# Kernel optimization log

Measured on AMD Instinct MI355X. Metric: run time of the kernel, lower is better.

The kernel has to match this reference:

```python
import jax, jax.numpy as jnp
import numpy as np

B, N, D = 8, 512, 16


def setup_inputs() -> dict:
    key = jax.random.key(0)
    k1, k2 = jax.random.split(key)
    # Fully-connected adjacency with diagonal = -1 (self is excluded as neighbor),
    # matching the tf.where(adj != -1) -> reshape [-1, N, N-1] pattern.
    adj_matrix = jnp.where(jnp.eye(N, dtype=bool)[None, :, :], -1, 1)
    adj_matrix = jnp.broadcast_to(adj_matrix, (B, N, N)).astype(jnp.int64)
    adj_coef = jax.random.normal(k1, (B, N, N), dtype=jnp.float32)
    neighbour_messages = jax.random.normal(k2, (B, N, D), dtype=jnp.float32)
    return {
        "adj_matrix": adj_matrix,
        "adj_coef": adj_coef,
        "neighbour_messages": neighbour_messages,
    }


def reference(adj_matrix, adj_coef, neighbour_messages):
    b, n, d = neighbour_messages.shape
    # tf.where(adj != -1) enumerates, per row i (in ascending column order), the
    # N-1 valid neighbor columns. Reproduce jit-safely: push invalid cols to the
    # end with sentinel n, sort, keep first n-1.
    cols = jnp.arange(n)[None, None, :]
    valid = adj_matrix != -1
    neighbor_idx = jnp.sort(jnp.where(valid, cols, n), axis=-1)[..., : n - 1]  # [B,N,N-1]
    # Batched gather: [B,N,N-1,D]
    gathered = neighbour_messages[jnp.arange(b)[:, None, None], neighbor_idx]
    # Concat self features with neighbor features along the 'slot' axis -> [B,N,N,D]
    updated = jnp.concatenate([neighbour_messages[:, :, None, :], gathered], axis=2)
    # Weight each slot by its adjacency coefficient, then flatten slots*features.
    updated = adj_coef[..., None] * updated
    return updated.reshape(b, n, n * d)
```

## Files before the change

### kernel.cpp

```cpp
#include <hip/hip_runtime.h>

#define NN 512
#define DD 16

__global__ __launch_bounds__(512) void graph_layer_kernel(
    const int*    __restrict__ adj,
    const float*  __restrict__ coef,
    const float4* __restrict__ msg4,
    float4*       __restrict__ out4)
{
    __shared__ float4 smsg[NN * 4];
    __shared__ float  scoef[NN];
    __shared__ int    snb[NN];
    __shared__ int    wtot[8];

    const int row  = blockIdx.x;
    const int b    = row >> 9;
    const int i    = row & (NN - 1);
    const int t    = threadIdx.x;
    const int lane = t & 63;
    const int wv   = t >> 6;

    scoef[t] = coef[(size_t)row * NN + t];

    {
        const float4* src = msg4 + (size_t)b * (NN * 4);
        #pragma unroll
        for (int k = 0; k < 4; ++k)
            smsg[t + k * 512] = src[t + k * 512];
    }

    const int  a     = adj[(size_t)row * NN + t];
    const bool valid = (a != -1);
    const unsigned long long m = __ballot(valid);
    const int  rank  = __popcll(m & ((1ULL << lane) - 1ULL));
    snb[t] = NN - 1;
    if (lane == 0) wtot[wv] = __popcll(m);
    __syncthreads();

    int base = 0;
    #pragma unroll
    for (int w = 0; w < 8; ++w)
        base += (w < wv) ? wtot[w] : 0;
    if (valid) {
        const int pos = base + rank;
        if (pos < NN) snb[pos] = t;
    }
    __syncthreads();

    float4* orow = out4 + (size_t)row * (NN * 4);
    #pragma unroll
    for (int k = 0; k < 4; ++k) {
        const int g = t + k * 512;
        const int j = g >> 2;
        const int q = g & 3;
        const int s = (j == 0) ? i : snb[j - 1];
        const float c = scoef[j];
        const float4 v = smsg[s * 4 + q];
        float4 o;
        o.x = c * v.x; o.y = c * v.y; o.z = c * v.z; o.w = c * v.w;
        orow[g] = o;
    }
}

extern "C" void kernel_launch(void* const* d_in, const int* in_sizes, int n_in,
                              void* d_out, int out_size, void* d_ws, size_t ws_size,
                              hipStream_t stream) {
    const int*    adj  = (const int*)d_in[0];
    const float*  coef = (const float*)d_in[1];
    const float4* msg4 = (const float4*)d_in[2];
    float4*       out4 = (float4*)d_out;

    const int B = 8;
    graph_layer_kernel<<<B * NN, 512, 0, stream>>>(adj, coef, msg4, out4);
}
```

Baseline: 155.2 us.

## Drop shared memory staging; compute neighbor index per thread via ballot masks and select-bit

Removes the shared-memory staging of messages, coefficients and the neighbor list, along with both block barriers. Each wave now builds all eight ballot masks of the adjacency row, and each thread locates its neighbor column with prefix counts and a bitwise select. Messages and coefficients are read straight from global memory (L2-cached), and output is written with nontemporal stores. The cost is redundant adjacency loads per wave and more per-thread ALU work, in exchange for no LDS traffic, no block-wide sync and higher occupancy.

```diff
diff --git a/kernel.cpp b/kernel.cpp
--- a/kernel.cpp
+++ b/kernel.cpp
@@ -1,75 +1,88 @@
 #include <hip/hip_runtime.h>
 
 #define NN 512
-#define DD 16
+
+typedef float f4 __attribute__((ext_vector_type(4)));
+
+__device__ __forceinline__ int select_bit(unsigned long long m, int k) {
+    int pos = 0;
+    unsigned int w = (unsigned int)m;
+    int c = __popc(w);
+    if (k >= c) { k -= c; pos = 32; w = (unsigned int)(m >> 32); }
+    unsigned int h = w & 0xFFFFu; c = __popc(h);
+    if (k >= c) { k -= c; pos += 16; w >>= 16; }
+    h = w & 0xFFu; c = __popc(h);
+    if (k >= c) { k -= c; pos += 8; w >>= 8; }
+    h = w & 0xFu; c = __popc(h);
+    if (k >= c) { k -= c; pos += 4; w >>= 4; }
+    h = w & 0x3u; c = __popc(h);
+    if (k >= c) { k -= c; pos += 2; w >>= 2; }
+    if (k >= (int)(w & 0x1u)) pos += 1;
+    return pos;
+}
 
 __global__ __launch_bounds__(512) void graph_layer_kernel(
-    const int*    __restrict__ adj,
-    const float*  __restrict__ coef,
-    const float4* __restrict__ msg4,
-    float4*       __restrict__ out4)
+    const int*   __restrict__ adj,
+    const float* __restrict__ coef,
+    const f4*    __restrict__ msg4,
+    f4*          __restrict__ out4)
 {
-    __shared__ float4 smsg[NN * 4];
-    __shared__ float  scoef[NN];
-    __shared__ int    snb[NN];
-    __shared__ int    wtot[8];
-
     const int row  = blockIdx.x;
     const int b    = row >> 9;
     const int i    = row & (NN - 1);
     const int t    = threadIdx.x;
     const int lane = t & 63;
-    const int wv   = t >> 6;
+    const size_t rowbase = (size_t)row * NN;
 
-    scoef[t] = coef[(size_t)row * NN + t];
+    unsigned long long mask[8];
+    #pragma unroll
+    for (int c = 0; c < 8; ++c)
+        mask[c] = __ballot(adj[rowbase + c * 64 + lane] != -1);
 
-    {
-        const float4* src = msg4 + (size_t)b * (NN * 4);
-        #pragma unroll
-        for (int k = 0; k < 4; ++k)
-            smsg[t + k * 512] = src[t + k * 512];
-    }
+    int cum[9];
+    cum[0] = 0;
+    #pragma unroll
+    for (int c = 0; c < 8; ++c) cum[c + 1] = cum[c] + __popcll(mask[c]);
 
-    const int  a     = adj[(size_t)row * NN + t];
-    const bool valid = (a != -1);
-    const unsigned long long m = __ballot(valid);
-    const int  rank  = __popcll(m & ((1ULL << lane) - 1ULL));
-    snb[t] = NN - 1;
-    if (lane == 0) wtot[wv] = __popcll(m);
-    __syncthreads();
+    const f4* msgb = msg4 + (size_t)b * (NN * 4);
+    f4*       orow = out4 + (size_t)row * (NN * 4);
+    const int q = t & 3;
 
-    int base = 0;
-    #pragma unroll
-    for (int w = 0; w < 8; ++w)
-        base += (w < wv) ? wtot[w] : 0;
-    if (valid) {
-        const int pos = base + rank;
-        if (pos < NN) snb[pos] = t;
-    }
-    __syncthreads();
-
-    float4* orow = out4 + (size_t)row * (NN * 4);
     #pragma unroll
     for (int k = 0; k < 4; ++k) {
         const int g = t + k * 512;
         const int j = g >> 2;
-        const int q = g & 3;
-        const int s = (j == 0) ? i : snb[j - 1];
-        const float c = scoef[j];
-        const float4 v = smsg[s * 4 + q];
-        float4 o;
-        o.x = c * v.x; o.y = c * v.y; o.z = c * v.z; o.w = c * v.w;
-        orow[g] = o;
+
+        int s;
+        if (j == 0) {
+            s = i;
+        } else {
+            const int p = j - 1;
+            if (p >= cum[8]) {
+                s = NN - 1;
+            } else {
+                int c = 0;
+                #pragma unroll
+                for (int cc = 1; cc < 8; ++cc) c += (p >= cum[cc]) ? 1 : 0;
+                s = c * 64 + select_bit(mask[c], p - cum[c]);
+            }
+        }
+
+        const float cv = coef[rowbase + j];
+        const f4    v  = msgb[s * 4 + q];
+        f4 o;
+        o.x = cv * v.x; o.y = cv * v.y; o.z = cv * v.z; o.w = cv * v.w;
+        __builtin_nontemporal_store(o, orow + g);
     }
 }
 
 extern "C" void kernel_launch(void* const* d_in, const int* in_sizes, int n_in,
                               void* d_out, int out_size, void* d_ws, size_t ws_size,
                               hipStream_t stream) {
-    const int*    adj  = (const int*)d_in[0];
-    const float*  coef = (const float*)d_in[1];
-    const float4* msg4 = (const float4*)d_in[2];
-    float4*       out4 = (float4*)d_out;
+    const int*   adj  = (const int*)d_in[0];
+    const float* coef = (const float*)d_in[1];
+    const f4*    msg4 = (const f4*)d_in[2];
+    f4*          out4 = (f4*)d_out;
 
     const int B = 8;
     graph_layer_kernel<<<B * NN, 512, 0, stream>>>(adj, coef, msg4, out4);
```

New measurement: 168.0 us. 8.2% more time.

## Split neighbor compaction and weighted write into two kernels with nontemporal stores

Applied to the files above, without the earlier changes.

The fused kernel becomes two kernels. The first compacts each row's valid neighbor indices (with the self index at slot 0) into a workspace buffer. The second reads those indices, the coefficients and the messages straight from global memory, with no shared-memory staging of the 32KB message block per row, and writes the output with nontemporal stores. The aim is to drop the per-block shared-memory fill and the barriers and to keep the large output stream out of the caches, at the cost of an extra kernel launch and a round trip of the index buffer through global memory.

```diff
diff --git a/kernel.cpp b/kernel.cpp
--- a/kernel.cpp
+++ b/kernel.cpp
@@ -1,76 +1,82 @@
 #include <hip/hip_runtime.h>
 
 #define NN 512
-#define DD 16
 
-__global__ __launch_bounds__(512) void graph_layer_kernel(
-    const int*    __restrict__ adj,
-    const float*  __restrict__ coef,
-    const float4* __restrict__ msg4,
-    float4*       __restrict__ out4)
+typedef float f4 __attribute__((ext_vector_type(4)));
+
+__global__ __launch_bounds__(512) void compact_kernel(
+    const int* __restrict__ adj,
+    int*       __restrict__ sidx)
 {
-    __shared__ float4 smsg[NN * 4];
-    __shared__ float  scoef[NN];
-    __shared__ int    snb[NN];
-    __shared__ int    wtot[8];
-
+    __shared__ int wtot[8];
     const int row  = blockIdx.x;
-    const int b    = row >> 9;
     const int i    = row & (NN - 1);
     const int t    = threadIdx.x;
     const int lane = t & 63;
     const int wv   = t >> 6;
 
-    scoef[t] = coef[(size_t)row * NN + t];
-
-    {
-        const float4* src = msg4 + (size_t)b * (NN * 4);
-        #pragma unroll
-        for (int k = 0; k < 4; ++k)
-            smsg[t + k * 512] = src[t + k * 512];
-    }
-
-    const int  a     = adj[(size_t)row * NN + t];
-    const bool valid = (a != -1);
+    const bool valid = (adj[(size_t)row * NN + t] != -1);
     const unsigned long long m = __ballot(valid);
-    const int  rank  = __popcll(m & ((1ULL << lane) - 1ULL));
-    snb[t] = NN - 1;
+    const int rank = __popcll(m & ((1ULL << lane) - 1ULL));
     if (lane == 0) wtot[wv] = __popcll(m);
     __syncthreads();
 
-    int base = 0;
+    int base = 0, V = 0;
     #pragma unroll
-    for (int w = 0; w < 8; ++w)
+    for (int w = 0; w < 8; ++w) {
         base += (w < wv) ? wtot[w] : 0;
+        V += wtot[w];
+    }
+
+    int* srow = sidx + (size_t)row * NN;
+    if (t == 0) srow[0] = i;
     if (valid) {
-        const int pos = base + rank;
-        if (pos < NN) snb[pos] = t;
+        const int pos = 1 + base + rank;
+        if (pos < NN) srow[pos] = t;
     }
-    __syncthreads();
+    if (t > V) srow[t] = NN - 1;
+}
 
-    float4* orow = out4 + (size_t)row * (NN * 4);
+__global__ __launch_bounds__(512) void write_kernel(
+    const int*   __restrict__ sidx,
+    const float* __restrict__ coef,
+    const f4*    __restrict__ msg4,
+    f4*          __restrict__ out4)
+{
+    const int row = blockIdx.x;
+    const int b   = row >> 9;
+    const int t   = threadIdx.x;
+    const size_t rowbase = (size_t)row * NN;
+
+    const int*   srow = sidx + rowbase;
+    const float* crow = coef + rowbase;
+    const f4*    msgb = msg4 + (size_t)b * (NN * 4);
+    f4*          orow = out4 + (size_t)row * (NN * 4);
+    const int q = t & 3;
+
     #pragma unroll
     for (int k = 0; k < 4; ++k) {
         const int g = t + k * 512;
         const int j = g >> 2;
-        const int q = g & 3;
-        const int s = (j == 0) ? i : snb[j - 1];
-        const float c = scoef[j];
-        const float4 v = smsg[s * 4 + q];
-        float4 o;
+        const int s = srow[j];
+        const float c = crow[j];
+        const f4    v = msgb[s * 4 + q];
+        f4 o;
         o.x = c * v.x; o.y = c * v.y; o.z = c * v.z; o.w = c * v.w;
-        orow[g] = o;
+        __builtin_nontemporal_store(o, orow + g);
     }
 }
 
 extern "C" void kernel_launch(void* const* d_in, const int* in_sizes, int n_in,
                               void* d_out, int out_size, void* d_ws, size_t ws_size,
                               hipStream_t stream) {
-    const int*    adj  = (const int*)d_in[0];
-    const float*  coef = (const float*)d_in[1];
-    const float4* msg4 = (const float4*)d_in[2];
-    float4*       out4 = (float4*)d_out;
+    const int*   adj  = (const int*)d_in[0];
+    const float* coef = (const float*)d_in[1];
+    const f4*    msg4 = (const f4*)d_in[2];
+    f4*          out4 = (f4*)d_out;
+    int*         sidx = (int*)d_ws;
 
     const int B = 8;
-    graph_layer_kernel<<<B * NN, 512, 0, stream>>>(adj, coef, msg4, out4);
+    compact_kernel<<<B * NN, 512, 0, stream>>>(adj, sidx);
+    write_kernel  <<<B * NN, 512, 0, stream>>>(sidx, coef, msg4, out4);
 }
```

Result: slower. 167.5 us (+7.9%).
